# Kernel optimization log

Hardware: AMD Instinct MI355X
Metric: run time of the kernel (lower is better)

Reference implementation:

```python
import jax, jax.numpy as jnp
import numpy as np


def _conv1d(x, w, b, pad):
    # x: (BN, Cin, L), w: (Cout, Cin, K) torch OIH layout
    y = jax.lax.conv_general_dilated(x, w, window_strides=(1,), padding=[(pad, pad)],
                                     dimension_numbers=('NCH', 'OIH', 'NCH'))
    return y + b[None, :, None]


def _mask_conv(m, k):
    # all-ones kernel conv then >=1 threshold (matches constant-init mask convs, no_grad)
    w = jnp.ones((1, 1, k), m.dtype)
    y = jax.lax.conv_general_dilated(m, w, window_strides=(1,), padding=[((k - 1) // 2, (k - 1) // 2)],
                                     dimension_numbers=('NCH', 'OIH', 'NCH'))
    return (y >= 1.0).astype(m.dtype)


def _branch(x, m, w1, b1, w2, b2, k):
    pad = (k - 1) // 2
    o = jax.nn.relu(_conv1d(x, w1, b1, pad))
    m = jax.lax.stop_gradient(_mask_conv(m, k))
    o = o * m
    o = jax.nn.relu(_conv1d(o, w2, b2, pad))
    m = jax.lax.stop_gradient(_mask_conv(m, k))
    return o * m


def _forward(all_xanes, all_xanes_mask, all_elem_info, all_elem_mask,
             w_b1c1, b_b1c1, w_b1c2, b_b1c2,
             w_b2c1, b_b2c1, w_b2c2, b_b2c2,
             w_b3c1, b_b3c1, w_b3c2, b_b3c2,
             w_xfc, b_xfc,
             w_float, b_float, atom_emb, type_emb,
             w_fuse, b_fuse,
             in_w, in_b, out_w, out_b,
             w_fc1, b_fc1, w_fc2, b_fc2):
    B, N, L = all_xanes.shape
    E, H = 64, 4
    dh = E // H
    # ---- MultiScaleXANESExtractor ----
    x = all_xanes.reshape(B * N, 1, L)
    m3 = jnp.broadcast_to(all_xanes_mask.reshape(B * N, 1, 1).astype(jnp.float32), (B * N, 1, L))
    o1 = _branch(x, m3, w_b1c1, b_b1c1, w_b1c2, b_b1c2, 3)
    o2 = _branch(x, m3, w_b2c1, b_b2c1, w_b2c2, b_b2c2, 5)
    o3 = _branch(x, m3, w_b3c1, b_b3c1, w_b3c2, b_b3c2, 7)
    cat = jnp.concatenate([o1, o2, o3], axis=1)  # (BN, 384, L)
    pooled = cat.reshape(B * N, 384, 10, L // 10).mean(-1).reshape(B * N, -1)  # AdaptiveAvgPool1d(10)
    xfeat = (pooled @ w_xfc.T + b_xfc).reshape(B, N, -1)  # (B, N, 32)
    valid = (m3.sum(axis=(1, 2)) > 0).astype(jnp.float32).reshape(B, N, 1)
    xfeat = xfeat * valid
    # ---- ElementsFeatureProcessor (vectorized gathers) ----
    maskf = all_elem_mask.astype(jnp.float32)
    masked = all_elem_info * maskf[..., None]
    ff = jax.nn.relu(masked[..., :5] @ w_float.T + b_float)  # (B, N, 16)
    an = masked[..., 5].astype(jnp.int32)
    et = masked[..., 6].astype(jnp.int32)
    valid_e = (maskf >= 0.5)
    inrange = (an >= 1) & (an <= 94)
    take = (valid_e & inrange).astype(jnp.float32)[..., None]
    ez = atom_emb[jnp.clip(an, 0, 94)] * take            # (B, N, 8)
    ety = type_emb[jnp.clip(et, 0, 5)] * take            # (B, N, 4)
    ff = ff * valid_e.astype(jnp.float32)[..., None]
    efeat = jnp.concatenate([ff, ez, ety], axis=-1) * maskf[..., None]  # (B, N, 28)
    # ---- FuseElementAndXANES ----
    fused = jnp.concatenate([xfeat, efeat], axis=-1) @ w_fuse.T + b_fuse
    fused = fused * maskf[..., None]  # (B, N, 64)
    # ---- AttentionAggregator (nn.MultiheadAttention, batch_first) ----
    qkv = fused @ in_w.T + in_b
    q, k, v = jnp.split(qkv, 3, axis=-1)
    q = q.reshape(B, N, H, dh)
    k = k.reshape(B, N, H, dh)
    v = v.reshape(B, N, H, dh)
    scores = jnp.einsum('bqhd,bkhd->bhqk', q, k) / jnp.sqrt(jnp.float32(dh))
    keymask = (maskf >= 0.5)
    scores = jnp.where(keymask[:, None, None, :], scores, jnp.float32(-1e30))
    attn = jax.nn.softmax(scores, axis=-1)
    ao = jnp.einsum('bhqk,bkhd->bqhd', attn, v).reshape(B, N, E)
    ao = ao @ out_w.T + out_b
    ao = ao * maskf[..., None]
    pooled2 = ao.sum(axis=1) / (maskf.sum(axis=1, keepdims=True) + 1e-8)
    h = jax.nn.relu(pooled2 @ w_fc1.T + b_fc1)
    return h @ w_fc2.T + b_fc2  # (B, num_classes)


def setup_inputs():
    key = jax.random.key(0)
    ks = jax.random.split(key, 40)
    B, N, L = 32, 16, 200
    all_xanes = jax.random.normal(ks[0], (B, N, L), jnp.float32)
    all_xanes_mask = jax.random.randint(ks[1], (B, N), 0, 2).astype(jnp.float32)
    ef = jax.random.normal(ks[2], (B, N, 7), jnp.float32)
    an = jax.random.randint(ks[3], (B, N), 1, 95).astype(jnp.float32)
    et = jax.random.randint(ks[4], (B, N), 0, 6).astype(jnp.float32)
    all_elem_info = ef.at[..., 5].set(an).at[..., 6].set(et)
    all_elem_mask = jax.random.randint(ks[5], (B, N), 0, 2).astype(jnp.float32)
    all_elem_mask = all_elem_mask.at[:, 0].set(1.0)  # avoid fully-padded rows (NaN softmax)

    def p(k, shape):
        return jax.random.normal(k, shape, jnp.float32) * 0.05

    inp = dict(all_xanes=all_xanes, all_xanes_mask=all_xanes_mask,
               all_elem_info=all_elem_info, all_elem_mask=all_elem_mask,
               w_b1c1=p(ks[6], (64, 1, 3)), b_b1c1=p(ks[7], (64,)),
               w_b1c2=p(ks[8], (128, 64, 3)), b_b1c2=p(ks[9], (128,)),
               w_b2c1=p(ks[10], (64, 1, 5)), b_b2c1=p(ks[11], (64,)),
               w_b2c2=p(ks[12], (128, 64, 5)), b_b2c2=p(ks[13], (128,)),
               w_b3c1=p(ks[14], (64, 1, 7)), b_b3c1=p(ks[15], (64,)),
               w_b3c2=p(ks[16], (128, 64, 7)), b_b3c2=p(ks[17], (128,)),
               w_xfc=p(ks[18], (32, 3840)), b_xfc=p(ks[19], (32,)),
               w_float=p(ks[20], (16, 5)), b_float=p(ks[21], (16,)),
               atom_emb=p(ks[22], (95, 8)), type_emb=p(ks[23], (6, 4)),
               w_fuse=p(ks[24], (64, 60)), b_fuse=p(ks[25], (64,)),
               in_w=p(ks[26], (192, 64)), in_b=p(ks[27], (192,)),
               out_w=p(ks[28], (64, 64)), out_b=p(ks[29], (64,)),
               w_fc1=p(ks[30], (64, 64)), b_fc1=p(ks[31], (64,)),
               w_fc2=p(ks[32], (1, 64)), b_fc2=p(ks[33], (1,)))
    return inp


def reference(all_xanes, all_xanes_mask, all_elem_info, all_elem_mask,
              w_b1c1, b_b1c1, w_b1c2, b_b1c2,
              w_b2c1, b_b2c1, w_b2c2, b_b2c2,
              w_b3c1, b_b3c1, w_b3c2, b_b3c2,
              w_xfc, b_xfc, w_float, b_float, atom_emb, type_emb,
              w_fuse, b_fuse, in_w, in_b, out_w, out_b,
              w_fc1, b_fc1, w_fc2, b_fc2):
    return _forward(all_xanes, all_xanes_mask, all_elem_info, all_elem_mask,
                    w_b1c1, b_b1c1, w_b1c2, b_b1c2,
                    w_b2c1, b_b2c1, w_b2c2, b_b2c2,
                    w_b3c1, b_b3c1, w_b3c2, b_b3c2,
                    w_xfc, b_xfc, w_float, b_float, atom_emb, type_emb,
                    w_fuse, b_fuse, in_w, in_b, out_w, out_b,
                    w_fc1, b_fc1, w_fc2, b_fc2)
```

## Files before the change

### kernel.cpp

```cpp
#include <hip/hip_runtime.h>
#include <math.h>

typedef float f32x4 __attribute__((ext_vector_type(4)));
typedef short short8 __attribute__((ext_vector_type(8)));

__device__ __forceinline__ short bf16r(float f) {
    union { float f; unsigned u; } x; x.f = f;
    unsigned u = x.u + 0x7fffu + ((x.u >> 16) & 1u);
    return (short)(u >> 16);
}

template<int K>
__device__ __forceinline__ void pack_branch(const float* __restrict__ w2,
                                            short* __restrict__ wpack, int u) {
    int lane = u & 63;
    int kb   = (u >> 6) & 1;
    int rem  = u >> 7;
    int j = rem % K, c = rem / K;
    int co  = c * 16 + (lane & 15);
    int cib = kb * 32 + 8 * ((lane >> 4) & 3);
    short8 v;
    #pragma unroll
    for (int i = 0; i < 8; ++i)
        v[i] = bf16r(w2[(co * 64 + (cib + i)) * K + j]);
    *reinterpret_cast<short8*>(wpack + (size_t)u * 8) = v;
}

__global__ __launch_bounds__(256) void pack_kernel(
    const float* __restrict__ w23, const float* __restrict__ w25,
    const float* __restrict__ w27,
    short* __restrict__ wp3, short* __restrict__ wp5, short* __restrict__ wp7)
{
    int tid = blockIdx.x * 256 + threadIdx.x;
    const int n3 = 8 * 3 * 2 * 64;
    const int n5 = 8 * 5 * 2 * 64;
    const int n7 = 8 * 7 * 2 * 64;
    if (tid < n3)                pack_branch<3>(w23, wp3, tid);
    else if (tid < n3 + n5)      pack_branch<5>(w25, wp5, tid - n3);
    else if (tid < n3 + n5 + n7) pack_branch<7>(w27, wp7, tid - n3 - n5);
}

template<int GV>
__device__ __forceinline__ void pool_accum(const f32x4* acc, float bb, float* pb) {
    #pragma unroll
    for (int lt = 0; lt < 13; ++lt) {
        #pragma unroll
        for (int r4 = 0; r4 < 4; ++r4) {
            const int l = lt * 16 + 4 * GV + r4;
            if (l < 200)
                pb[l / 20] += fmaxf(acc[lt][r4] + bb, 0.0f);
        }
    }
}

template<int K>
__device__ __forceinline__ void branch_body(
    const int bn, const int t,
    const float* __restrict__ x, const float* __restrict__ xmask,
    const float* __restrict__ w1, const float* __restrict__ b1,
    const float* __restrict__ b2, const short* __restrict__ wpack,
    float* __restrict__ pooled_g, int br,
    float* xs, short* t1s, float* pooled_s, float* b2s)
{
    constexpr int PAD = (K - 1) / 2;
    const int lane = t & 63;
    const int w    = t >> 6;
    const int lane15 = lane & 15;
    const int g      = (lane >> 4) & 3;

    if (xmask[bn] == 0.0f) return;

    if (t < 208) xs[t] = 0.0f;
    for (int idx = t; idx < 32 * 64; idx += 512) {
        int rr = idx >> 6;
        int row = (rr < 3) ? rr : (200 + rr);
        t1s[row * 64 + (idx & 63)] = 0;
    }
    if (t < 128) b2s[t] = b2[t];
    __syncthreads();

    if (t < 200) xs[3 + t] = x[bn * 200 + t];
    __syncthreads();

    {
        float w1_0 = w1[lane * K + 0], w1_1 = w1[lane * K + 1], w1_2 = w1[lane * K + 2];
        float w1_3 = 0.f, w1_4 = 0.f, w1_5 = 0.f, w1_6 = 0.f;
        if (K > 3) { w1_3 = w1[lane * K + 3]; w1_4 = w1[lane * K + 4]; }
        if (K > 5) { w1_5 = w1[lane * K + 5]; w1_6 = w1[lane * K + 6]; }
        const float b1r = b1[lane];
        for (int l = w; l < 200; l += 8) {
            const float* xp = &xs[3 + l - PAD];
            float a = b1r;
            a = fmaf(w1_0, xp[0], a);
            a = fmaf(w1_1, xp[1], a);
            a = fmaf(w1_2, xp[2], a);
            if (K > 3) { a = fmaf(w1_3, xp[3], a); a = fmaf(w1_4, xp[4], a); }
            if (K > 5) { a = fmaf(w1_5, xp[5], a); a = fmaf(w1_6, xp[6], a); }
            const int row = l + 3;
            t1s[row * 64 + (lane ^ ((row & 7) << 3))] = bf16r(fmaxf(a, 0.0f));
        }
    }
    __syncthreads();

    const int co = w * 16 + lane15;
    const float bb = b2s[co];
    f32x4 acc[13];
    #pragma unroll
    for (int lt = 0; lt < 13; ++lt) {
        f32x4 z = {0.f, 0.f, 0.f, 0.f};
        acc[lt] = z;
    }
    {
        const short* wpB = wpack + ((size_t)(w * 2 * K) * 64 + lane) * 8;
        #pragma unroll
        for (int j = 0; j < K; ++j) {
            #pragma unroll
            for (int kb = 0; kb < 2; ++kb) {
                const short8 bfr = *reinterpret_cast<const short8*>(
                    wpB + (size_t)(j * 2 + kb) * 64 * 8);
                const int r0  = lane15 + 3 + j - PAD;
                const int col = (kb * 32 + 8 * g) ^ ((r0 & 7) << 3);
                const short* abase = &t1s[r0 * 64 + col];
                #pragma unroll
                for (int lt = 0; lt < 13; ++lt) {
                    acc[lt] = __builtin_amdgcn_mfma_f32_16x16x32_bf16(
                        *reinterpret_cast<const short8*>(abase + lt * 1024),
                        bfr, acc[lt], 0, 0, 0);
                }
            }
        }
    }

    {
        float pb[10];
        #pragma unroll
        for (int b = 0; b < 10; ++b) pb[b] = 0.0f;
        if      (g == 0) pool_accum<0>(acc, bb, pb);
        else if (g == 1) pool_accum<1>(acc, bb, pb);
        else if (g == 2) pool_accum<2>(acc, bb, pb);
        else             pool_accum<3>(acc, bb, pb);
        #pragma unroll
        for (int b = 0; b < 10; ++b) {
            pb[b] += __shfl_xor(pb[b], 16);
            pb[b] += __shfl_xor(pb[b], 32);
        }
        if (lane < 16) {
            #pragma unroll
            for (int b = 0; b < 10; ++b)
                pooled_s[co * 12 + b] = pb[b];
        }
    }
    __syncthreads();

    for (int idx = t; idx < 1280; idx += 512) {
        int co2 = idx / 10, bin = idx - co2 * 10;
        pooled_g[bn * 3840 + br * 1280 + idx] = pooled_s[co2 * 12 + bin] * 0.05f;
    }
}

__global__ __launch_bounds__(512) void branch_fused(
    const float* __restrict__ x, const float* __restrict__ xmask,
    const float* __restrict__ w1_3, const float* __restrict__ b1_3,
    const float* __restrict__ b2_3, const short* __restrict__ wp3,
    const float* __restrict__ w1_5, const float* __restrict__ b1_5,
    const float* __restrict__ b2_5, const short* __restrict__ wp5,
    const float* __restrict__ w1_7, const float* __restrict__ b1_7,
    const float* __restrict__ b2_7, const short* __restrict__ wp7,
    float* __restrict__ pooled_g)
{
    __shared__ float xs[208];
    __shared__ short t1s[232 * 64];
    __shared__ float pooled_s[128 * 12];
    __shared__ float b2s[128];

    const int bn = blockIdx.x;
    const int br = blockIdx.y;
    const int t  = threadIdx.x;

    if (br == 0)
        branch_body<3>(bn, t, x, xmask, w1_3, b1_3, b2_3, wp3, pooled_g, 0,
                       xs, t1s, pooled_s, b2s);
    else if (br == 1)
        branch_body<5>(bn, t, x, xmask, w1_5, b1_5, b2_5, wp5, pooled_g, 1,
                       xs, t1s, pooled_s, b2s);
    else
        branch_body<7>(bn, t, x, xmask, w1_7, b1_7, b2_7, wp7, pooled_g, 2,
                       xs, t1s, pooled_s, b2s);
}

__global__ __launch_bounds__(256) void xfc_kernel(
    const float* __restrict__ pooled,
    const float* __restrict__ w_xfc,
    const float* __restrict__ b_xfc,
    const float* __restrict__ xmask,
    float* __restrict__ xfeat)
{
    const int bn   = blockIdx.x;
    const int t    = threadIdx.x;
    const int lane = t & 63;
    const int ww   = t >> 6;
    __shared__ f32x4 prow4[960];
    const f32x4* pr4 = reinterpret_cast<const f32x4*>(pooled + bn * 3840);
    for (int i = t; i < 960; i += 256) prow4[i] = pr4[i];
    __syncthreads();

    const float m = xmask[bn];
    #pragma unroll
    for (int k = 0; k < 8; ++k) {
        const int o = ww * 8 + k;
        const f32x4* wr4 = reinterpret_cast<const f32x4*>(w_xfc + o * 3840) + lane;
        float a0 = 0.0f, a1 = 0.0f;
        #pragma unroll
        for (int it = 0; it < 15; ++it) {
            const f32x4 wv = wr4[it * 64];
            const f32x4 pv = prow4[it * 64 + lane];
            float s = wv[0] * pv[0];
            s = fmaf(wv[1], pv[1], s);
            s = fmaf(wv[2], pv[2], s);
            s = fmaf(wv[3], pv[3], s);
            if (it & 1) a1 += s; else a0 += s;
        }
        float a = a0 + a1;
        #pragma unroll
        for (int d = 32; d >= 1; d >>= 1) a += __shfl_xor(a, d);
        if (lane == 0) xfeat[bn * 32 + o] = (a + b_xfc[o]) * m;
    }
}

__global__ __launch_bounds__(256) void tail_kernel(
    const float* __restrict__ xfeat,
    const float* __restrict__ elem_info,
    const float* __restrict__ emaskp,
    const float* __restrict__ w_float, const float* __restrict__ b_float,
    const float* __restrict__ atom_emb, const float* __restrict__ type_emb,
    const float* __restrict__ w_fuse,  const float* __restrict__ b_fuse,
    const float* __restrict__ in_w,    const float* __restrict__ in_b,
    const float* __restrict__ out_w,   const float* __restrict__ out_b,
    const float* __restrict__ w_fc1,   const float* __restrict__ b_fc1,
    const float* __restrict__ w_fc2,   const float* __restrict__ b_fc2,
    float* __restrict__ out)
{
    const int b = blockIdx.x;
    const int t = threadIdx.x;

    __shared__ float fu[16][60];
    __shared__ float fused[16][64];
    __shared__ float qkvs[16][192];
    __shared__ float sc[4][16][16];
    __shared__ float ao[16][64];
    __shared__ float aoo[16][64];
    __shared__ float p2s[64];
    __shared__ float hs[64];
    __shared__ float em[16];

    if (t < 16) em[t] = emaskp[b * 16 + t];
    for (int d = t; d < 512; d += 256) {
        int n = d >> 5, o = d & 31;
        fu[n][o] = xfeat[(b * 16 + n) * 32 + o];
    }
    __syncthreads();

    {
        int n = t >> 4, slot = t & 15;
        float m  = em[n];
        float vE = (m >= 0.5f) ? 1.0f : 0.0f;
        const float* ei = elem_info + (b * 16 + n) * 7;
        float a = b_float[slot];
        #pragma unroll
        for (int i = 0; i < 5; ++i)
            a = fmaf(ei[i] * m, w_float[slot * 5 + i], a);
        fu[n][32 + slot] = fmaxf(a, 0.0f) * vE * m;

        int an = (int)(ei[5] * m);
        int et = (int)(ei[6] * m);
        float take = (vE != 0.0f && an >= 1 && an <= 94) ? 1.0f : 0.0f;
        int anc = an < 0 ? 0 : (an > 94 ? 94 : an);
        int etc = et < 0 ? 0 : (et > 5 ? 5 : et);
        if (slot < 8)
            fu[n][48 + slot] = atom_emb[anc * 8 + slot] * take * m;
        else if (slot < 12)
            fu[n][56 + (slot - 8)] = type_emb[etc * 4 + (slot - 8)] * take * m;
    }
    __syncthreads();

    for (int d = t; d < 1024; d += 256) {
        int n = d >> 6, o = d & 63;
        float a = b_fuse[o];
        const float* wr = w_fuse + o * 60;
        #pragma unroll
        for (int i = 0; i < 60; ++i) a = fmaf(fu[n][i], wr[i], a);
        fused[n][o] = a * em[n];
    }
    __syncthreads();

    for (int d = t; d < 3072; d += 256) {
        int n = d / 192, rr = d - n * 192;
        float a = in_b[rr];
        const float* wr = in_w + rr * 64;
        #pragma unroll
        for (int i = 0; i < 64; ++i) a = fmaf(fused[n][i], wr[i], a);
        qkvs[n][rr] = a;
    }
    __syncthreads();

    for (int d = t; d < 1024; d += 256) {
        int h = d >> 8, i = (d >> 4) & 15, j = d & 15;
        float a = 0.0f;
        #pragma unroll
        for (int dd = 0; dd < 16; ++dd)
            a = fmaf(qkvs[i][h * 16 + dd], qkvs[j][64 + h * 16 + dd], a);
        a *= 0.25f;
        if (em[j] < 0.5f) a = -1e30f;
        sc[h][i][j] = a;
    }
    __syncthreads();

    if (t < 64) {
        int h = t >> 4, i = t & 15;
        float mx = -3.4e38f;
        #pragma unroll
        for (int j = 0; j < 16; ++j) mx = fmaxf(mx, sc[h][i][j]);
        float e[16];
        float s = 0.0f;
        #pragma unroll
        for (int j = 0; j < 16; ++j) { e[j] = expf(sc[h][i][j] - mx); s += e[j]; }
        float inv = 1.0f / s;
        #pragma unroll
        for (int j = 0; j < 16; ++j) sc[h][i][j] = e[j] * inv;
    }
    __syncthreads();

    for (int d = t; d < 1024; d += 256) {
        int n = d >> 6, e = d & 63, h = e >> 4;
        float a = 0.0f;
        #pragma unroll
        for (int j = 0; j < 16; ++j)
            a = fmaf(sc[h][n][j], qkvs[j][128 + e], a);
        ao[n][e] = a;
    }
    __syncthreads();

    for (int d = t; d < 1024; d += 256) {
        int n = d >> 6, o = d & 63;
        float a = out_b[o];
        const float* wr = out_w + o * 64;
        #pragma unroll
        for (int i = 0; i < 64; ++i) a = fmaf(ao[n][i], wr[i], a);
        aoo[n][o] = a * em[n];
    }
    __syncthreads();

    if (t < 64) {
        float s = 0.0f, ms = 0.0f;
        #pragma unroll
        for (int n = 0; n < 16; ++n) { s += aoo[n][t]; ms += em[n]; }
        p2s[t] = s / (ms + 1e-8f);
    }
    __syncthreads();

    if (t < 64) {
        float a = b_fc1[t];
        const float* wr = w_fc1 + t * 64;
        #pragma unroll
        for (int i = 0; i < 64; ++i) a = fmaf(p2s[i], wr[i], a);
        hs[t] = fmaxf(a, 0.0f);
    }
    __syncthreads();

    if (t < 64) {
        float v = hs[t] * w_fc2[t];
        #pragma unroll
        for (int d2 = 32; d2 >= 1; d2 >>= 1) v += __shfl_xor(v, d2);
        if (t == 0) out[b] = v + b_fc2[0];
    }
}

extern "C" void kernel_launch(void* const* d_in, const int* in_sizes, int n_in,
                              void* d_out, int out_size, void* d_ws, size_t ws_size,
                              hipStream_t stream)
{
    (void)in_sizes; (void)n_in; (void)out_size; (void)ws_size;
    const float* x     = (const float*)d_in[0];
    const float* xmask = (const float*)d_in[1];
    const float* einfo = (const float*)d_in[2];
    const float* emask = (const float*)d_in[3];

    float* pooled = (float*)d_ws;
    float* xfeat  = pooled + 512 * 3840;
    short* wp3 = (short*)(xfeat + 512 * 32);
    short* wp5 = wp3 + 24576;
    short* wp7 = wp5 + 40960;

    pack_kernel<<<60, 256, 0, stream>>>(
        (const float*)d_in[6], (const float*)d_in[10], (const float*)d_in[14],
        wp3, wp5, wp7);

    branch_fused<<<dim3(512, 3), 512, 0, stream>>>(x, xmask,
        (const float*)d_in[4],  (const float*)d_in[5],  (const float*)d_in[7],  wp3,
        (const float*)d_in[8],  (const float*)d_in[9],  (const float*)d_in[11], wp5,
        (const float*)d_in[12], (const float*)d_in[13], (const float*)d_in[15], wp7,
        pooled);

    xfc_kernel<<<512, 256, 0, stream>>>(pooled,
        (const float*)d_in[16], (const float*)d_in[17], xmask, xfeat);

    tail_kernel<<<32, 256, 0, stream>>>(xfeat, einfo, emask,
        (const float*)d_in[18], (const float*)d_in[19],
        (const float*)d_in[20], (const float*)d_in[21],
        (const float*)d_in[22], (const float*)d_in[23],
        (const float*)d_in[24], (const float*)d_in[25],
        (const float*)d_in[26], (const float*)d_in[27],
        (const float*)d_in[28], (const float*)d_in[29],
        (const float*)d_in[30], (const float*)d_in[31],
        (float*)d_out);
}
```

Before: 83.19 us.

## Fuse xfc linear layer into branch kernel epilogue with per-branch partial sums

Each branch block now multiplies its pooled tile in shared memory by its slice of w_xfc and writes 32 partial outputs per branch, instead of storing the full pooled tensor to global memory. The separate xfc kernel is removed. The tail kernel sums the three partials, adds the bias and applies the mask. This drops one launch and the large pooled write/read round trip. In exchange every branch block re-reads its w_xfc slice with a strided access pattern and does a short reduction at the end of the block.

```diff
diff --git a/kernel.cpp b/kernel.cpp
--- a/kernel.cpp
+++ b/kernel.cpp
@@ -59,7 +59,7 @@
     const float* __restrict__ x, const float* __restrict__ xmask,
     const float* __restrict__ w1, const float* __restrict__ b1,
     const float* __restrict__ b2, const short* __restrict__ wpack,
-    float* __restrict__ pooled_g, int br,
+    const float* __restrict__ w_xfc, float* __restrict__ xfeatP, int br,
     float* xs, short* t1s, float* pooled_s, float* b2s)
 {
     constexpr int PAD = (K - 1) / 2;
@@ -152,9 +152,23 @@
     }
     __syncthreads();
 
-    for (int idx = t; idx < 1280; idx += 512) {
-        int co2 = idx / 10, bin = idx - co2 * 10;
-        pooled_g[bn * 3840 + br * 1280 + idx] = pooled_s[co2 * 12 + bin] * 0.05f;
+    {
+        const int o = t >> 4;
+        const int part = t & 15;
+        const float* wr = w_xfc + o * 3840 + br * 1280;
+        float a = 0.0f;
+        #pragma unroll
+        for (int k = 0; k < 8; ++k) {
+            const int co2 = part + 16 * k;
+            #pragma unroll
+            for (int bin = 0; bin < 10; ++bin)
+                a = fmaf(pooled_s[co2 * 12 + bin], wr[co2 * 10 + bin], a);
+        }
+        a += __shfl_xor(a, 1);
+        a += __shfl_xor(a, 2);
+        a += __shfl_xor(a, 4);
+        a += __shfl_xor(a, 8);
+        if (part == 0) xfeatP[(br * 512 + bn) * 32 + o] = a * 0.05f;
     }
 }
 
@@ -166,7 +180,7 @@
     const float* __restrict__ b2_5, const short* __restrict__ wp5,
     const float* __restrict__ w1_7, const float* __restrict__ b1_7,
     const float* __restrict__ b2_7, const short* __restrict__ wp7,
-    float* __restrict__ pooled_g)
+    const float* __restrict__ w_xfc, float* __restrict__ xfeatP)
 {
     __shared__ float xs[208];
     __shared__ short t1s[232 * 64];
@@ -178,57 +192,20 @@
     const int t  = threadIdx.x;
 
     if (br == 0)
-        branch_body<3>(bn, t, x, xmask, w1_3, b1_3, b2_3, wp3, pooled_g, 0,
+        branch_body<3>(bn, t, x, xmask, w1_3, b1_3, b2_3, wp3, w_xfc, xfeatP, 0,
                        xs, t1s, pooled_s, b2s);
     else if (br == 1)
-        branch_body<5>(bn, t, x, xmask, w1_5, b1_5, b2_5, wp5, pooled_g, 1,
+        branch_body<5>(bn, t, x, xmask, w1_5, b1_5, b2_5, wp5, w_xfc, xfeatP, 1,
                        xs, t1s, pooled_s, b2s);
     else
-        branch_body<7>(bn, t, x, xmask, w1_7, b1_7, b2_7, wp7, pooled_g, 2,
+        branch_body<7>(bn, t, x, xmask, w1_7, b1_7, b2_7, wp7, w_xfc, xfeatP, 2,
                        xs, t1s, pooled_s, b2s);
 }
 
-__global__ __launch_bounds__(256) void xfc_kernel(
-    const float* __restrict__ pooled,
-    const float* __restrict__ w_xfc,
+__global__ __launch_bounds__(256) void tail_kernel(
+    const float* __restrict__ xfeatP,
     const float* __restrict__ b_xfc,
-    const float* __restrict__ xmask,
-    float* __restrict__ xfeat)
-{
-    const int bn   = blockIdx.x;
-    const int t    = threadIdx.x;
-    const int lane = t & 63;
-    const int ww   = t >> 6;
-    __shared__ f32x4 prow4[960];
-    const f32x4* pr4 = reinterpret_cast<const f32x4*>(pooled + bn * 3840);
-    for (int i = t; i < 960; i += 256) prow4[i] = pr4[i];
-    __syncthreads();
-
-    const float m = xmask[bn];
-    #pragma unroll
-    for (int k = 0; k < 8; ++k) {
-        const int o = ww * 8 + k;
-        const f32x4* wr4 = reinterpret_cast<const f32x4*>(w_xfc + o * 3840) + lane;
-        float a0 = 0.0f, a1 = 0.0f;
-        #pragma unroll
-        for (int it = 0; it < 15; ++it) {
-            const f32x4 wv = wr4[it * 64];
-            const f32x4 pv = prow4[it * 64 + lane];
-            float s = wv[0] * pv[0];
-            s = fmaf(wv[1], pv[1], s);
-            s = fmaf(wv[2], pv[2], s);
-            s = fmaf(wv[3], pv[3], s);
-            if (it & 1) a1 += s; else a0 += s;
-        }
-        float a = a0 + a1;
-        #pragma unroll
-        for (int d = 32; d >= 1; d >>= 1) a += __shfl_xor(a, d);
-        if (lane == 0) xfeat[bn * 32 + o] = (a + b_xfc[o]) * m;
-    }
-}
-
-__global__ __launch_bounds__(256) void tail_kernel(
-    const float* __restrict__ xfeat,
+    const float* __restrict__ xmaskp,
     const float* __restrict__ elem_info,
     const float* __restrict__ emaskp,
     const float* __restrict__ w_float, const float* __restrict__ b_float,
@@ -256,7 +233,11 @@
     if (t < 16) em[t] = emaskp[b * 16 + t];
     for (int d = t; d < 512; d += 256) {
         int n = d >> 5, o = d & 31;
-        fu[n][o] = xfeat[(b * 16 + n) * 32 + o];
+        const int bn = b * 16 + n;
+        float a = xfeatP[bn * 32 + o]
+                + xfeatP[(512 + bn) * 32 + o]
+                + xfeatP[(1024 + bn) * 32 + o];
+        fu[n][o] = (a + b_xfc[o]) * xmaskp[bn];
     }
     __syncthreads();
 
@@ -385,9 +366,8 @@
     const float* einfo = (const float*)d_in[2];
     const float* emask = (const float*)d_in[3];
 
-    float* pooled = (float*)d_ws;
-    float* xfeat  = pooled + 512 * 3840;
-    short* wp3 = (short*)(xfeat + 512 * 32);
+    float* xfeatP = (float*)d_ws;
+    short* wp3 = (short*)(xfeatP + 3 * 512 * 32);
     short* wp5 = wp3 + 24576;
     short* wp7 = wp5 + 40960;
 
@@ -399,12 +379,10 @@
         (const float*)d_in[4],  (const float*)d_in[5],  (const float*)d_in[7],  wp3,
         (const float*)d_in[8],  (const float*)d_in[9],  (const float*)d_in[11], wp5,
         (const float*)d_in[12], (const float*)d_in[13], (const float*)d_in[15], wp7,
-        pooled);
-
-    xfc_kernel<<<512, 256, 0, stream>>>(pooled,
-        (const float*)d_in[16], (const float*)d_in[17], xmask, xfeat);
-
-    tail_kernel<<<32, 256, 0, stream>>>(xfeat, einfo, emask,
+        (const float*)d_in[16], xfeatP);
+
+    tail_kernel<<<32, 256, 0, stream>>>(xfeatP,
+        (const float*)d_in[17], xmask, einfo, emask,
         (const float*)d_in[18], (const float*)d_in[19],
         (const float*)d_in[20], (const float*)d_in[21],
         (const float*)d_in[22], (const float*)d_in[23],
```

Result: slower. 87.99 us (+5.8%).
